# Optimization experiments

Hardware: AMD Instinct MI355X
Metric: run time of the kernel (lower is better)

The kernel has to match this reference:

```python
import jax, jax.numpy as jnp
import numpy as np

B, T, H, F = 32, 2048, 1024, 1024  # batch, kv_len, hidden_size, feature_size


def setup_inputs() -> dict:
    key = jax.random.key(0)
    ks = jax.random.split(key, 6)
    s = 0.02  # param init scale
    return {
        "query": jax.random.normal(ks[0], (B, 1, H), jnp.float32),
        "keys": jax.random.normal(ks[1], (B, T, F), jnp.float32),
        "Wa_w": jax.random.normal(ks[2], (H, H), jnp.float32) * s,
        "Wa_b": jnp.zeros((H,), jnp.float32),
        "Ua_w": jax.random.normal(ks[3], (H, F), jnp.float32) * s,
        "Ua_b": jnp.zeros((H,), jnp.float32),
        "Va_w": jax.random.normal(ks[4], (1, H), jnp.float32) * s,
        "Va_b": jnp.zeros((1,), jnp.float32),
    }


def reference(query, keys, Wa_w, Wa_b, Ua_w, Ua_b, Va_w, Va_b):
    # Wa(query): [B,1,H]; Ua(keys): [B,T,H]
    q = jnp.einsum('bqh,oh->bqo', query, Wa_w) + Wa_b
    k = jnp.einsum('btf,of->bto', keys, Ua_w) + Ua_b
    e = jnp.tanh(q + k)                                   # [B,T,H] (broadcast over q dim of size 1)
    scores = jnp.einsum('bth,h->bt', e, Va_w[0]) + Va_b[0]  # Va(...).squeeze(2) -> [B,T]
    scores = scores[:, None, :]                           # unsqueeze(1) -> [B,1,T]
    weights = jax.nn.softmax(scores, axis=-1)             # [B,1,T]
    context = jnp.einsum('bqt,btf->bqf', weights, keys)   # bmm -> [B,1,F]
    return context, weights
```

## Files before the change

### kernel.cpp

```cpp
#include <hip/hip_runtime.h>
#include <hip/hip_bf16.h>

typedef float  f32x4 __attribute__((ext_vector_type(4)));
typedef short  s16x8 __attribute__((ext_vector_type(8)));
typedef __hip_bfloat16 bf16;

#define BDIM 32
#define TDIM 2048
#define HDIM 1024
#define FDIM 1024
#define MTOT (BDIM*TDIM)

#define GLOAD16(gp, lp) __builtin_amdgcn_global_load_lds(                     \
    (const __attribute__((address_space(1))) void*)(gp),                      \
    (__attribute__((address_space(3))) void*)(lp), 16, 0, 0)

__global__ __launch_bounds__(256) void cvt_bf16_kernel(
    const float* __restrict__ src, bf16* __restrict__ dst, int n8)
{
    int i = blockIdx.x * 256 + threadIdx.x;
    const int stride = gridDim.x * 256;
    for (; i < n8; i += stride) {
        const f32x4 a = ((const f32x4*)src)[2 * i];
        const f32x4 b = ((const f32x4*)src)[2 * i + 1];
        union { bf16 h[8]; s16x8 v; } u;
        #pragma unroll
        for (int j = 0; j < 4; ++j) {
            u.h[j]     = __float2bfloat16(a[j]);
            u.h[4 + j] = __float2bfloat16(b[j]);
        }
        ((s16x8*)dst)[i] = u.v;
    }
}

__global__ __launch_bounds__(256) void qeff_kernel(
    const float* __restrict__ query, const float* __restrict__ Wa_w,
    const float* __restrict__ Wa_b,  const float* __restrict__ Ua_b,
    float* __restrict__ qe)
{
    const int lane = threadIdx.x & 63;
    const int gw   = blockIdx.x * 4 + (threadIdx.x >> 6);
    const int b    = gw >> 10;
    const int o    = gw & 1023;
    const float* qp = query + (size_t)b * HDIM;
    const float* wp = Wa_w  + (size_t)o * HDIM;
    float s = 0.f;
    #pragma unroll
    for (int i = 0; i < 16; ++i) {
        const int h = i * 64 + lane;
        s += qp[h] * wp[h];
    }
    #pragma unroll
    for (int off = 32; off > 0; off >>= 1) s += __shfl_down(s, off);
    if (lane == 0) qe[gw] = s + Wa_b[o] + Ua_b[o];
}

__global__ __launch_bounds__(256) void score_gemm_bf16_kernel(
    const bf16* __restrict__ Ab, const bf16* __restrict__ Bb,
    const float* __restrict__ qe, const float* __restrict__ Va,
    float* __restrict__ scores)
{
    __shared__ bf16 As[128 * 32];
    __shared__ bf16 Bs[128 * 32];

    const int tid  = threadIdx.x;
    const int lane = tid & 63;
    const int wid  = tid >> 6;
    const int wr   = wid >> 1, wc = wid & 1;

    const int g     = blockIdx.x;
    const int local = g >> 3;
    const int mt    = (g & 7) * 64 + (local >> 3);
    const int nt    = local & 7;
    const int m0 = mt * 128;
    const int n0 = nt * 128;

    f32x4 acc[4][4];
    #pragma unroll
    for (int m = 0; m < 4; ++m)
        #pragma unroll
        for (int n = 0; n < 4; ++n) acc[m][n] = (f32x4){0.f, 0.f, 0.f, 0.f};

    for (int kt = 0; kt < 32; ++kt) {
        __syncthreads();
        const int k0 = kt * 32;
        #pragma unroll
        for (int i = 0; i < 2; ++i) {
            const int c = i * 256 + tid;
            const int r = c >> 2, j = c & 3;
            const int basec = i * 256 + wid * 64;
            GLOAD16(Ab + (size_t)(m0 + r) * FDIM + k0 + j * 8, As + basec * 8);
            GLOAD16(Bb + (size_t)(n0 + r) * FDIM + k0 + j * 8, Bs + basec * 8);
        }
        __syncthreads();

        s16x8 af[4], bfr[4];
        const int q = lane >> 4, rr = lane & 15;
        #pragma unroll
        for (int m = 0; m < 4; ++m)
            af[m] = *(const s16x8*)&As[(wr * 64 + m * 16 + rr) * 32 + q * 8];
        #pragma unroll
        for (int n = 0; n < 4; ++n)
            bfr[n] = *(const s16x8*)&Bs[(wc * 64 + n * 16 + rr) * 32 + q * 8];
        #pragma unroll
        for (int m = 0; m < 4; ++m)
            #pragma unroll
            for (int n = 0; n < 4; ++n)
                acc[m][n] = __builtin_amdgcn_mfma_f32_16x16x32_bf16(
                    af[m], bfr[n], acc[m][n], 0, 0, 0);
    }

    const int b = m0 >> 11;
    const float* qrow = qe + (size_t)b * HDIM;
    #pragma unroll
    for (int m = 0; m < 4; ++m) {
        float part[4] = {0.f, 0.f, 0.f, 0.f};
        #pragma unroll
        for (int n = 0; n < 4; ++n) {
            const int c    = n0 + wc * 64 + n * 16 + (lane & 15);
            const float va = Va[c];
            const float qv = qrow[c];
            #pragma unroll
            for (int j = 0; j < 4; ++j) {
                const float x = qv + acc[m][n][j];
                const float e = __expf(2.0f * x);
                part[j] += va * (1.0f - 2.0f / (e + 1.0f));
            }
        }
        #pragma unroll
        for (int j = 0; j < 4; ++j)
            #pragma unroll
            for (int off = 1; off < 16; off <<= 1)
                part[j] += __shfl_xor(part[j], off);
        if ((lane & 15) == 0) {
            const int r = m0 + wr * 64 + m * 16 + (lane >> 4) * 4;
            #pragma unroll
            for (int j = 0; j < 4; ++j) atomicAdd(&scores[r + j], part[j]);
        }
    }
}

__global__ __launch_bounds__(256) void score_gemm_f32_kernel(
    const float* __restrict__ keys, const float* __restrict__ Ua,
    const float* __restrict__ qe,   const float* __restrict__ Va,
    float* __restrict__ scores)
{
    __shared__ bf16 As[128][40];
    __shared__ bf16 Bs[128][40];

    const int tid  = threadIdx.x;
    const int lane = tid & 63;
    const int wid  = tid >> 6;
    const int wr   = wid >> 1, wc = wid & 1;
    const int n0   = blockIdx.x * 128;
    const int m0   = blockIdx.y * 128;

    const int srow  = tid >> 1;
    const int shalf = tid & 1;
    const float* gA = keys + (size_t)(m0 + srow) * FDIM + shalf * 16;
    const float* gB = Ua   + (size_t)(n0 + srow) * FDIM + shalf * 16;

    f32x4 acc[4][4];
    #pragma unroll
    for (int m = 0; m < 4; ++m)
        #pragma unroll
        for (int n = 0; n < 4; ++n) acc[m][n] = (f32x4){0.f, 0.f, 0.f, 0.f};

    float4 ra[4], rb[4];
    #pragma unroll
    for (int i = 0; i < 4; ++i) {
        ra[i] = ((const float4*)gA)[i];
        rb[i] = ((const float4*)gB)[i];
    }

    for (int kt = 0; kt < 32; ++kt) {
        __syncthreads();
        {
            union { bf16 h[16]; s16x8 v[2]; } ua, ub;
            #pragma unroll
            for (int i = 0; i < 4; ++i) {
                const float* fa = (const float*)&ra[i];
                const float* fb = (const float*)&rb[i];
                #pragma unroll
                for (int j = 0; j < 4; ++j) {
                    ua.h[i*4+j] = __float2bfloat16(fa[j]);
                    ub.h[i*4+j] = __float2bfloat16(fb[j]);
                }
            }
            *(s16x8*)&As[srow][shalf*16]     = ua.v[0];
            *(s16x8*)&As[srow][shalf*16 + 8] = ua.v[1];
            *(s16x8*)&Bs[srow][shalf*16]     = ub.v[0];
            *(s16x8*)&Bs[srow][shalf*16 + 8] = ub.v[1];
        }
        __syncthreads();

        if (kt + 1 < 32) {
            const float* pa = gA + (kt + 1) * 32;
            const float* pb = gB + (kt + 1) * 32;
            #pragma unroll
            for (int i = 0; i < 4; ++i) {
                ra[i] = ((const float4*)pa)[i];
                rb[i] = ((const float4*)pb)[i];
            }
        }

        s16x8 af[4], bfr[4];
        #pragma unroll
        for (int m = 0; m < 4; ++m)
            af[m] = *(const s16x8*)&As[wr*64 + m*16 + (lane & 15)][(lane >> 4) * 8];
        #pragma unroll
        for (int n = 0; n < 4; ++n)
            bfr[n] = *(const s16x8*)&Bs[wc*64 + n*16 + (lane & 15)][(lane >> 4) * 8];
        #pragma unroll
        for (int m = 0; m < 4; ++m)
            #pragma unroll
            for (int n = 0; n < 4; ++n)
                acc[m][n] = __builtin_amdgcn_mfma_f32_16x16x32_bf16(
                    af[m], bfr[n], acc[m][n], 0, 0, 0);
    }

    const int b = m0 >> 11;
    const float* qrow = qe + (size_t)b * HDIM;
    #pragma unroll
    for (int m = 0; m < 4; ++m) {
        float part[4] = {0.f, 0.f, 0.f, 0.f};
        #pragma unroll
        for (int n = 0; n < 4; ++n) {
            const int c    = n0 + wc*64 + n*16 + (lane & 15);
            const float va = Va[c];
            const float qv = qrow[c];
            #pragma unroll
            for (int j = 0; j < 4; ++j) {
                const float x = qv + acc[m][n][j];
                const float e = __expf(2.0f * x);
                part[j] += va * (1.0f - 2.0f / (e + 1.0f));
            }
        }
        #pragma unroll
        for (int j = 0; j < 4; ++j)
            #pragma unroll
            for (int off = 1; off < 16; off <<= 1)
                part[j] += __shfl_xor(part[j], off);
        if ((lane & 15) == 0) {
            const int r = m0 + wr*64 + m*16 + (lane >> 4) * 4;
            #pragma unroll
            for (int j = 0; j < 4; ++j) atomicAdd(&scores[r + j], part[j]);
        }
    }
}

__global__ __launch_bounds__(256) void softmax_kernel(float* __restrict__ sw)
{
    const int b    = blockIdx.x;
    const int tid  = threadIdx.x;
    const int lane = tid & 63, wid = tid >> 6;
    __shared__ float red[8];

    float v[8];
    float m = -3.4e38f;
    #pragma unroll
    for (int i = 0; i < 8; ++i) {
        v[i] = sw[b * TDIM + i * 256 + tid];
        m = fmaxf(m, v[i]);
    }
    #pragma unroll
    for (int off = 32; off > 0; off >>= 1) m = fmaxf(m, __shfl_xor(m, off));
    if (lane == 0) red[wid] = m;
    __syncthreads();
    m = fmaxf(fmaxf(red[0], red[1]), fmaxf(red[2], red[3]));

    float s = 0.f;
    #pragma unroll
    for (int i = 0; i < 8; ++i) { v[i] = __expf(v[i] - m); s += v[i]; }
    #pragma unroll
    for (int off = 32; off > 0; off >>= 1) s += __shfl_xor(s, off);
    if (lane == 0) red[4 + wid] = s;
    __syncthreads();
    s = (red[4] + red[5]) + (red[6] + red[7]);

    const float inv = 1.0f / s;
    #pragma unroll
    for (int i = 0; i < 8; ++i) sw[b * TDIM + i * 256 + tid] = v[i] * inv;
}

__global__ __launch_bounds__(256) void context_bf16_kernel(
    const bf16* __restrict__ keys, const float* __restrict__ w,
    float* __restrict__ ctx)
{
    const int tc  = blockIdx.x;
    const int b   = blockIdx.y;
    const int tid = threadIdx.x;
    __shared__ float ws_[128];
    if (tid < 128) ws_[tid] = w[b * TDIM + tc * 128 + tid];
    __syncthreads();

    const bf16* kp = keys + ((size_t)b * TDIM + (size_t)tc * 128) * FDIM + tid * 4;
    float4 acc = {0.f, 0.f, 0.f, 0.f};
    #pragma unroll 8
    for (int t = 0; t < 128; ++t) {
        const short4 kv = *(const short4*)(kp + (size_t)t * FDIM);
        const float wt = ws_[t];
        acc.x += wt * __uint_as_float(((unsigned)(unsigned short)kv.x) << 16);
        acc.y += wt * __uint_as_float(((unsigned)(unsigned short)kv.y) << 16);
        acc.z += wt * __uint_as_float(((unsigned)(unsigned short)kv.z) << 16);
        acc.w += wt * __uint_as_float(((unsigned)(unsigned short)kv.w) << 16);
    }
    float* cp = ctx + (size_t)b * FDIM + tid * 4;
    atomicAdd(cp + 0, acc.x); atomicAdd(cp + 1, acc.y);
    atomicAdd(cp + 2, acc.z); atomicAdd(cp + 3, acc.w);
}

__global__ __launch_bounds__(256) void context_f32_kernel(
    const float* __restrict__ keys, const float* __restrict__ w,
    float* __restrict__ ctx)
{
    const int tc  = blockIdx.x;
    const int b   = blockIdx.y;
    const int tid = threadIdx.x;
    __shared__ float ws_[128];
    if (tid < 128) ws_[tid] = w[b * TDIM + tc * 128 + tid];
    __syncthreads();

    const float* kp = keys + ((size_t)b * TDIM + (size_t)tc * 128) * FDIM + tid * 4;
    float4 acc = {0.f, 0.f, 0.f, 0.f};
    #pragma unroll 8
    for (int t = 0; t < 128; ++t) {
        const float4 kv = *(const float4*)(kp + (size_t)t * FDIM);
        const float wt = ws_[t];
        acc.x += wt * kv.x; acc.y += wt * kv.y;
        acc.z += wt * kv.z; acc.w += wt * kv.w;
    }
    float* cp = ctx + (size_t)b * FDIM + tid * 4;
    atomicAdd(cp + 0, acc.x); atomicAdd(cp + 1, acc.y);
    atomicAdd(cp + 2, acc.z); atomicAdd(cp + 3, acc.w);
}

extern "C" void kernel_launch(void* const* d_in, const int* in_sizes, int n_in,
                              void* d_out, int out_size, void* d_ws, size_t ws_size,
                              hipStream_t stream)
{
    const float* query = (const float*)d_in[0];
    const float* keys  = (const float*)d_in[1];
    const float* Wa_w  = (const float*)d_in[2];
    const float* Wa_b  = (const float*)d_in[3];
    const float* Ua_w  = (const float*)d_in[4];
    const float* Ua_b  = (const float*)d_in[5];
    const float* Va_w  = (const float*)d_in[6];

    float* out = (float*)d_out;
    float* ctx = out;
    float* sw  = out + BDIM * HDIM;

    const size_t needA = (size_t)MTOT * FDIM * sizeof(bf16);
    const size_t needB = (size_t)HDIM * FDIM * sizeof(bf16);
    const bool fast = ws_size >= needA + needB;

    hipMemsetAsync(sw, 0, (size_t)BDIM * TDIM * sizeof(float), stream);
    qeff_kernel<<<dim3(BDIM * HDIM / 4), 256, 0, stream>>>(query, Wa_w, Wa_b, Ua_b, ctx);

    if (fast) {
        bf16* Ab = (bf16*)d_ws;
        bf16* Bb = Ab + (size_t)MTOT * FDIM;
        cvt_bf16_kernel<<<dim3(2048), 256, 0, stream>>>(keys, Ab, MTOT * FDIM / 8);
        cvt_bf16_kernel<<<dim3(512),  256, 0, stream>>>(Ua_w, Bb, HDIM * FDIM / 8);
        score_gemm_bf16_kernel<<<dim3(4096), 256, 0, stream>>>(Ab, Bb, ctx, Va_w, sw);
        softmax_kernel<<<dim3(BDIM), 256, 0, stream>>>(sw);
        hipMemsetAsync(ctx, 0, (size_t)BDIM * HDIM * sizeof(float), stream);
        context_bf16_kernel<<<dim3(16, BDIM), 256, 0, stream>>>(Ab, sw, ctx);
    } else {
        score_gemm_f32_kernel<<<dim3(HDIM / 128, MTOT / 128), 256, 0, stream>>>(
            keys, Ua_w, ctx, Va_w, sw);
        softmax_kernel<<<dim3(BDIM), 256, 0, stream>>>(sw);
        hipMemsetAsync(ctx, 0, (size_t)BDIM * HDIM * sizeof(float), stream);
        context_f32_kernel<<<dim3(16, BDIM), 256, 0, stream>>>(keys, sw, ctx);
    }
}
```

Baseline: 309.3 us.

## Rewrite bf16 score GEMM as 256x256 double-buffered, swizzled 8-wave kernel

Replaces the 128x128 single-buffered bf16 score GEMM with a 256x256 tile kernel of 512 threads that uses a K-step of 64, double-buffered LDS filled by direct global-to-LDS loads, and an XOR-swizzled layout to avoid bank conflicts. The MFMA work is split into four phases interleaved with fragment reads and next-tile prefetch, with s_setprio raising priority around the matrix ops. The goal is to raise arithmetic intensity and overlap memory with compute in the dominant GEMM. In exchange it uses 128KB of LDS and far more registers per block, which could limit occupancy or cause register spills.

```diff
diff --git a/kernel.cpp b/kernel.cpp
--- a/kernel.cpp
+++ b/kernel.cpp
@@ -55,74 +55,160 @@
     if (lane == 0) qe[gw] = s + Wa_b[o] + Ua_b[o];
 }
 
-__global__ __launch_bounds__(256) void score_gemm_bf16_kernel(
+#define STAGE_A(buf_, kb_, h_, s_) GLOAD16(                                    \
+    Ab + (size_t)(M0 + (h_)*128 + (((s_)>>1)<<4) + srow) * FDIM               \
+       + (kb_) + (((s_)&1)<<5) + scg*8,                                        \
+    &As[buf_][((((h_)*8 + ((s_)>>1)) * 2 + ((s_)&1)) << 9)])
+#define STAGE_B(buf_, kb_, h_, s_) GLOAD16(                                    \
+    Bb + (size_t)(N0 + (h_)*128 + (((s_)>>1)<<4) + srow) * FDIM               \
+       + (kb_) + (((s_)&1)<<5) + scg*8,                                        \
+    &Bs[buf_][((((h_)*8 + ((s_)>>1)) * 2 + ((s_)&1)) << 9)])
+
+__global__ __launch_bounds__(512, 2) void score_gemm_256_kernel(
     const bf16* __restrict__ Ab, const bf16* __restrict__ Bb,
     const float* __restrict__ qe, const float* __restrict__ Va,
     float* __restrict__ scores)
 {
-    __shared__ bf16 As[128 * 32];
-    __shared__ bf16 Bs[128 * 32];
+    __shared__ bf16 As[2][16384];
+    __shared__ bf16 Bs[2][16384];
 
     const int tid  = threadIdx.x;
     const int lane = tid & 63;
-    const int wid  = tid >> 6;
-    const int wr   = wid >> 1, wc = wid & 1;
-
-    const int g     = blockIdx.x;
-    const int local = g >> 3;
-    const int mt    = (g & 7) * 64 + (local >> 3);
-    const int nt    = local & 7;
-    const int m0 = mt * 128;
-    const int n0 = nt * 128;
-
-    f32x4 acc[4][4];
-    #pragma unroll
-    for (int m = 0; m < 4; ++m)
+    const int w    = tid >> 6;
+    const int wr   = w >> 2;
+    const int wc   = w & 3;
+
+    const int bid   = blockIdx.x;
+    const int local = bid >> 3;
+    const int mt    = (bid & 7) * 32 + (local >> 2);
+    const int nt    = local & 3;
+    const int M0 = mt * 256, N0 = nt * 256;
+
+    const int srow = lane >> 2;
+    const int scg  = (lane & 3) ^ ((lane >> 4) & 3);
+    const int r    = lane & 15;
+    const int roff = r * 32 + (((lane >> 4) ^ ((r >> 2) & 3)) & 3) * 8;
+
+    f32x4 acc[8][4];
+    #pragma unroll
+    for (int m = 0; m < 8; ++m)
         #pragma unroll
         for (int n = 0; n < 4; ++n) acc[m][n] = (f32x4){0.f, 0.f, 0.f, 0.f};
 
-    for (int kt = 0; kt < 32; ++kt) {
-        __syncthreads();
-        const int k0 = kt * 32;
-        #pragma unroll
-        for (int i = 0; i < 2; ++i) {
-            const int c = i * 256 + tid;
-            const int r = c >> 2, j = c & 3;
-            const int basec = i * 256 + wid * 64;
-            GLOAD16(Ab + (size_t)(m0 + r) * FDIM + k0 + j * 8, As + basec * 8);
-            GLOAD16(Bb + (size_t)(n0 + r) * FDIM + k0 + j * 8, Bs + basec * 8);
-        }
-        __syncthreads();
-
-        s16x8 af[4], bfr[4];
-        const int q = lane >> 4, rr = lane & 15;
-        #pragma unroll
-        for (int m = 0; m < 4; ++m)
-            af[m] = *(const s16x8*)&As[(wr * 64 + m * 16 + rr) * 32 + q * 8];
-        #pragma unroll
-        for (int n = 0; n < 4; ++n)
-            bfr[n] = *(const s16x8*)&Bs[(wc * 64 + n * 16 + rr) * 32 + q * 8];
-        #pragma unroll
-        for (int m = 0; m < 4; ++m)
-            #pragma unroll
-            for (int n = 0; n < 4; ++n)
-                acc[m][n] = __builtin_amdgcn_mfma_f32_16x16x32_bf16(
-                    af[m], bfr[n], acc[m][n], 0, 0, 0);
-    }
-
-    const int b = m0 >> 11;
+    STAGE_A(0, 0, 0, w); STAGE_A(0, 0, 0, w + 8);
+    STAGE_A(0, 0, 1, w); STAGE_A(0, 0, 1, w + 8);
+    STAGE_B(0, 0, 0, w); STAGE_B(0, 0, 0, w + 8);
+    STAGE_B(0, 0, 1, w); STAGE_B(0, 0, 1, w + 8);
+    asm volatile("s_waitcnt vmcnt(0)" ::: "memory");
+    __builtin_amdgcn_s_barrier();
+
+    for (int t = 0; t < 16; ++t) {
+        const int rb  = t & 1, wbuf = rb ^ 1;
+        const int kt1 = (t + 1) << 6;
+        const bool pf = (t + 1 < 16);
+
+        s16x8 a[4][2];
+        s16x8 bq[4][2];
+
+        #pragma unroll
+        for (int mf = 0; mf < 4; ++mf)
+            #pragma unroll
+            for (int ks = 0; ks < 2; ++ks)
+                a[mf][ks] = *(const s16x8*)
+                    &As[rb][(((wr * 8 + mf) * 2 + ks) << 9) + roff];
+        #pragma unroll
+        for (int nf = 0; nf < 2; ++nf)
+            #pragma unroll
+            for (int ks = 0; ks < 2; ++ks)
+                bq[nf][ks] = *(const s16x8*)
+                    &Bs[rb][(((wc * 4 + nf) * 2 + ks) << 9) + roff];
+        if (pf) {
+            STAGE_A(wbuf, kt1, 0, w); STAGE_A(wbuf, kt1, 0, w + 8);
+            STAGE_A(wbuf, kt1, 1, w); STAGE_A(wbuf, kt1, 1, w + 8);
+        }
+        __builtin_amdgcn_s_barrier();
+        __builtin_amdgcn_s_setprio(1);
+        #pragma unroll
+        for (int mf = 0; mf < 4; ++mf)
+            #pragma unroll
+            for (int nf = 0; nf < 2; ++nf)
+                #pragma unroll
+                for (int ks = 0; ks < 2; ++ks)
+                    acc[mf][nf] = __builtin_amdgcn_mfma_f32_16x16x32_bf16(
+                        a[mf][ks], bq[nf][ks], acc[mf][nf], 0, 0, 0);
+        __builtin_amdgcn_s_setprio(0);
+        __builtin_amdgcn_s_barrier();
+
+        #pragma unroll
+        for (int nf = 2; nf < 4; ++nf)
+            #pragma unroll
+            for (int ks = 0; ks < 2; ++ks)
+                bq[nf][ks] = *(const s16x8*)
+                    &Bs[rb][(((wc * 4 + nf) * 2 + ks) << 9) + roff];
+        if (pf) {
+            STAGE_B(wbuf, kt1, 0, w); STAGE_B(wbuf, kt1, 0, w + 8);
+            STAGE_B(wbuf, kt1, 1, w); STAGE_B(wbuf, kt1, 1, w + 8);
+        }
+        __builtin_amdgcn_s_barrier();
+        __builtin_amdgcn_s_setprio(1);
+        #pragma unroll
+        for (int mf = 0; mf < 4; ++mf)
+            #pragma unroll
+            for (int nf = 2; nf < 4; ++nf)
+                #pragma unroll
+                for (int ks = 0; ks < 2; ++ks)
+                    acc[mf][nf] = __builtin_amdgcn_mfma_f32_16x16x32_bf16(
+                        a[mf][ks], bq[nf][ks], acc[mf][nf], 0, 0, 0);
+        __builtin_amdgcn_s_setprio(0);
+        __builtin_amdgcn_s_barrier();
+
+        #pragma unroll
+        for (int mf = 0; mf < 4; ++mf)
+            #pragma unroll
+            for (int ks = 0; ks < 2; ++ks)
+                a[mf][ks] = *(const s16x8*)
+                    &As[rb][(((wr * 8 + 4 + mf) * 2 + ks) << 9) + roff];
+        __builtin_amdgcn_s_barrier();
+        __builtin_amdgcn_s_setprio(1);
+        #pragma unroll
+        for (int mf = 0; mf < 4; ++mf)
+            #pragma unroll
+            for (int nf = 2; nf < 4; ++nf)
+                #pragma unroll
+                for (int ks = 0; ks < 2; ++ks)
+                    acc[4 + mf][nf] = __builtin_amdgcn_mfma_f32_16x16x32_bf16(
+                        a[mf][ks], bq[nf][ks], acc[4 + mf][nf], 0, 0, 0);
+        __builtin_amdgcn_s_setprio(0);
+        __builtin_amdgcn_s_barrier();
+
+        __builtin_amdgcn_s_setprio(1);
+        #pragma unroll
+        for (int mf = 0; mf < 4; ++mf)
+            #pragma unroll
+            for (int nf = 0; nf < 2; ++nf)
+                #pragma unroll
+                for (int ks = 0; ks < 2; ++ks)
+                    acc[4 + mf][nf] = __builtin_amdgcn_mfma_f32_16x16x32_bf16(
+                        a[mf][ks], bq[nf][ks], acc[4 + mf][nf], 0, 0, 0);
+        __builtin_amdgcn_s_setprio(0);
+        asm volatile("s_waitcnt vmcnt(0)" ::: "memory");
+        __builtin_amdgcn_s_barrier();
+        __builtin_amdgcn_sched_barrier(0);
+    }
+
+    const int b = M0 >> 11;
     const float* qrow = qe + (size_t)b * HDIM;
     #pragma unroll
-    for (int m = 0; m < 4; ++m) {
+    for (int mf = 0; mf < 8; ++mf) {
         float part[4] = {0.f, 0.f, 0.f, 0.f};
         #pragma unroll
-        for (int n = 0; n < 4; ++n) {
-            const int c    = n0 + wc * 64 + n * 16 + (lane & 15);
+        for (int nf = 0; nf < 4; ++nf) {
+            const int c    = N0 + wc * 64 + nf * 16 + (lane & 15);
             const float va = Va[c];
             const float qv = qrow[c];
             #pragma unroll
             for (int j = 0; j < 4; ++j) {
-                const float x = qv + acc[m][n][j];
+                const float x = qv + acc[mf][nf][j];
                 const float e = __expf(2.0f * x);
                 part[j] += va * (1.0f - 2.0f / (e + 1.0f));
             }
@@ -133,9 +219,9 @@
             for (int off = 1; off < 16; off <<= 1)
                 part[j] += __shfl_xor(part[j], off);
         if ((lane & 15) == 0) {
-            const int r = m0 + wr * 64 + m * 16 + (lane >> 4) * 4;
-            #pragma unroll
-            for (int j = 0; j < 4; ++j) atomicAdd(&scores[r + j], part[j]);
+            const int rr = M0 + wr * 128 + mf * 16 + (lane >> 4) * 4;
+            #pragma unroll
+            for (int j = 0; j < 4; ++j) atomicAdd(&scores[rr + j], part[j]);
         }
     }
 }
@@ -145,8 +231,8 @@
     const float* __restrict__ qe,   const float* __restrict__ Va,
     float* __restrict__ scores)
 {
-    __shared__ bf16 As[128][40];
-    __shared__ bf16 Bs[128][40];
+    __shared__ bf16 Asf[128][40];
+    __shared__ bf16 Bsf[128][40];
 
     const int tid  = threadIdx.x;
     const int lane = tid & 63;
@@ -166,11 +252,11 @@
         #pragma unroll
         for (int n = 0; n < 4; ++n) acc[m][n] = (f32x4){0.f, 0.f, 0.f, 0.f};
 
-    float4 ra[4], rb[4];
+    float4 ra[4], rbv[4];
     #pragma unroll
     for (int i = 0; i < 4; ++i) {
-        ra[i] = ((const float4*)gA)[i];
-        rb[i] = ((const float4*)gB)[i];
+        ra[i]  = ((const float4*)gA)[i];
+        rbv[i] = ((const float4*)gB)[i];
     }
 
     for (int kt = 0; kt < 32; ++kt) {
@@ -180,17 +266,17 @@
             #pragma unroll
             for (int i = 0; i < 4; ++i) {
                 const float* fa = (const float*)&ra[i];
-                const float* fb = (const float*)&rb[i];
+                const float* fb = (const float*)&rbv[i];
                 #pragma unroll
                 for (int j = 0; j < 4; ++j) {
                     ua.h[i*4+j] = __float2bfloat16(fa[j]);
                     ub.h[i*4+j] = __float2bfloat16(fb[j]);
                 }
             }
-            *(s16x8*)&As[srow][shalf*16]     = ua.v[0];
-            *(s16x8*)&As[srow][shalf*16 + 8] = ua.v[1];
-            *(s16x8*)&Bs[srow][shalf*16]     = ub.v[0];
-            *(s16x8*)&Bs[srow][shalf*16 + 8] = ub.v[1];
+            *(s16x8*)&Asf[srow][shalf*16]     = ua.v[0];
+            *(s16x8*)&Asf[srow][shalf*16 + 8] = ua.v[1];
+            *(s16x8*)&Bsf[srow][shalf*16]     = ub.v[0];
+            *(s16x8*)&Bsf[srow][shalf*16 + 8] = ub.v[1];
         }
         __syncthreads();
 
@@ -199,18 +285,18 @@
             const float* pb = gB + (kt + 1) * 32;
             #pragma unroll
             for (int i = 0; i < 4; ++i) {
-                ra[i] = ((const float4*)pa)[i];
-                rb[i] = ((const float4*)pb)[i];
+                ra[i]  = ((const float4*)pa)[i];
+                rbv[i] = ((const float4*)pb)[i];
             }
         }
 
         s16x8 af[4], bfr[4];
         #pragma unroll
         for (int m = 0; m < 4; ++m)
-            af[m] = *(const s16x8*)&As[wr*64 + m*16 + (lane & 15)][(lane >> 4) * 8];
+            af[m] = *(const s16x8*)&Asf[wr*64 + m*16 + (lane & 15)][(lane >> 4) * 8];
         #pragma unroll
         for (int n = 0; n < 4; ++n)
-            bfr[n] = *(const s16x8*)&Bs[wc*64 + n*16 + (lane & 15)][(lane >> 4) * 8];
+            bfr[n] = *(const s16x8*)&Bsf[wc*64 + n*16 + (lane & 15)][(lane >> 4) * 8];
         #pragma unroll
         for (int m = 0; m < 4; ++m)
             #pragma unroll
@@ -242,9 +328,9 @@
             for (int off = 1; off < 16; off <<= 1)
                 part[j] += __shfl_xor(part[j], off);
         if ((lane & 15) == 0) {
-            const int r = m0 + wr*64 + m*16 + (lane >> 4) * 4;
-            #pragma unroll
-            for (int j = 0; j < 4; ++j) atomicAdd(&scores[r + j], part[j]);
+            const int rr = m0 + wr*64 + m*16 + (lane >> 4) * 4;
+            #pragma unroll
+            for (int j = 0; j < 4; ++j) atomicAdd(&scores[rr + j], part[j]);
         }
     }
 }
@@ -363,7 +449,7 @@
         bf16* Bb = Ab + (size_t)MTOT * FDIM;
         cvt_bf16_kernel<<<dim3(2048), 256, 0, stream>>>(keys, Ab, MTOT * FDIM / 8);
         cvt_bf16_kernel<<<dim3(512),  256, 0, stream>>>(Ua_w, Bb, HDIM * FDIM / 8);
-        score_gemm_bf16_kernel<<<dim3(4096), 256, 0, stream>>>(Ab, Bb, ctx, Va_w, sw);
+        score_gemm_256_kernel<<<dim3(1024), 512, 0, stream>>>(Ab, Bb, ctx, Va_w, sw);
         softmax_kernel<<<dim3(BDIM), 256, 0, stream>>>(sw);
         hipMemsetAsync(ctx, 0, (size_t)BDIM * HDIM * sizeof(float), stream);
         context_bf16_kernel<<<dim3(16, BDIM), 256, 0, stream>>>(Ab, sw, ctx);
```

After: 285.8 us. 1.08x faster.
